# Kernel tuning notes

Hardware: AMD Instinct MI355X
Metric: run time of the kernel (lower is better)

The kernel has to match this reference:

```python
import jax, jax.numpy as jnp
import numpy as np

WS = 8                      # window_size
N = WS * WS                 # 64, Householder dimension
PAD = WS - 1                # reflect-pad total (7)
PAD_LO, PAD_HI = PAD // 2, PAD - PAD // 2  # (3, 4)


def setup_inputs() -> dict:
    key = jax.random.key(0)
    k1, k2 = jax.random.split(key)
    x = jax.random.normal(k1, (2, 8, 256, 256), dtype=jnp.float32)
    v = jax.random.normal(k2, (N, N), dtype=jnp.float32)  # 64 Householder vectors (rows)
    return {"x": x, "v": v}


def _get_A(v):
    # A = prod_i (I - 2 v_i v_i^T / ||v_i||^2), composed left-to-right as in the torch loop.
    # A @ (I - 2 v v^T / s) == A - (2/s) * (A v) v^T  -> rank-1 update per step.
    n = v.shape[-1]
    def step(A, vi):
        s = jnp.sum(vi * vi)
        Av = A @ vi                      # [n]
        return A - (2.0 / s) * jnp.outer(Av, vi), None
    A, _ = jax.lax.scan(step, jnp.eye(n, dtype=v.dtype), v)
    return A


def reference(x, v):
    b, c, H, W = x.shape
    xi = x.reshape(b * c, 1, H, W)
    # reflect padding (3,4) on both spatial dims, as in F.pad(..., mode='reflect')
    xp = jnp.pad(xi, ((0, 0), (0, 0), (PAD_LO, PAD_HI), (PAD_LO, PAD_HI)), mode='reflect')
    # unfold: kernel=8, stride=1, padding=0 -> [bc, 64, H, W] (C=1 so channel ordering matches torch)
    patches = jax.lax.conv_general_dilated_patches(
        xp, filter_shape=(WS, WS), window_strides=(1, 1), padding='VALID')
    cols = patches.reshape(b * c, N, H * W)          # [bc, 64, L]
    A = _get_A(v)                                     # [64, 64]
    # OrthoT1d(dim=1): transpose(1,-1) @ A, transpose back -> out[b,m,l] = sum_k cols[b,k,l] A[k,m]
    out = jnp.einsum('bkl,km->bml', cols, A)          # [bc, 64, L]
    # rearrange 'b (h w) (k1 k2) -> b (h w) k1 k2' with k1=H, k2=W
    return out.reshape(b * c, N, H, W)
```

## Files before the change

### kernel.cpp

```cpp
#include <hip/hip_runtime.h>

#define HSZ 256
#define WSZ 256
#define BC  16
#define NCH 64
#define PADLO 3

#define TW 64
#define TH 8
#define NTHR 256
#define TR 15
#define TC 71
#define TSTRIDE 80

typedef short bf16x8 __attribute__((ext_vector_type(8)));
typedef float f32x4  __attribute__((ext_vector_type(4)));

__device__ __forceinline__ int reflect_idx(int i) {
    i = (i < 0) ? -i : i;
    i = (i >= HSZ) ? (2 * (HSZ - 1) - i) : i;
    return i;
}

__device__ __forceinline__ unsigned short f2bf(float f) {
    unsigned u = __builtin_bit_cast(unsigned, f);
    u += 0x7FFFu + ((u >> 16) & 1u);
    return (unsigned short)(u >> 16);
}

__global__ void build_A_frags(const float* __restrict__ v,
                              unsigned short* __restrict__ frags) {
    __shared__ float As[64][64];
    const int t = threadIdx.x;
    const int w = t >> 6;
    const int l = t & 63;
    const int r = (w << 4) | (l & 15);
    const int q = l >> 4;

    float row[16];
#pragma unroll
    for (int c = 0; c < 16; ++c) row[c] = (q * 16 + c == r) ? 1.0f : 0.0f;

    for (int i = 0; i < 64; ++i) {
        const f32x4* vp = (const f32x4*)(v + i * 64 + q * 16);
        f32x4 v0 = vp[0], v1 = vp[1], v2 = vp[2], v3 = vp[3];
        float vv[16];
#pragma unroll
        for (int j = 0; j < 4; ++j) { vv[j] = v0[j]; vv[4+j] = v1[j]; vv[8+j] = v2[j]; vv[12+j] = v3[j]; }

        float s0 = 0, s1 = 0, s2 = 0, s3 = 0, a0 = 0, a1 = 0, a2 = 0, a3 = 0;
#pragma unroll
        for (int c = 0; c < 4; ++c) {
            s0 = fmaf(vv[c],      vv[c],      s0);
            s1 = fmaf(vv[4+c],    vv[4+c],    s1);
            s2 = fmaf(vv[8+c],    vv[8+c],    s2);
            s3 = fmaf(vv[12+c],   vv[12+c],   s3);
            a0 = fmaf(row[c],     vv[c],      a0);
            a1 = fmaf(row[4+c],   vv[4+c],    a1);
            a2 = fmaf(row[8+c],   vv[8+c],    a2);
            a3 = fmaf(row[12+c],  vv[12+c],   a3);
        }
        float s  = (s0 + s1) + (s2 + s3);
        float av = (a0 + a1) + (a2 + a3);
        av += __shfl_xor(av, 16); s += __shfl_xor(s, 16);
        av += __shfl_xor(av, 32); s += __shfl_xor(s, 32);

        const float scale = 2.0f * av / s;
#pragma unroll
        for (int c = 0; c < 16; ++c) row[c] = fmaf(-scale, vv[c], row[c]);
    }
#pragma unroll
    for (int c = 0; c < 16; ++c) As[r][q * 16 + c] = row[c];
    __syncthreads();

    const int ln = l & 15, lh = l >> 4;
    const int mb = w;
#pragma unroll
    for (int c2 = 0; c2 < 2; ++c2)
#pragma unroll
        for (int j = 0; j < 8; ++j) {
            float val = As[c2 * 32 + lh * 8 + j][mb * 16 + ln];
            frags[(((mb * 2 + c2) * 64) + l) * 8 + j] = f2bf(val);
        }
}

__global__ __launch_bounds__(256)
void ortho_mfma_kernel(const float* __restrict__ x,
                       const unsigned short* __restrict__ frags,
                       float* __restrict__ out) {
    __shared__ float tile[TR][TSTRIDE];

    const int b  = blockIdx.z;
    const int y0 = blockIdx.y * TH;
    const int x0 = blockIdx.x * TW;
    const float* __restrict__ xb = x + (size_t)b * (HSZ * WSZ);

    const int tx = threadIdx.x;
    const int ty = threadIdx.y;
    const int tid = ty * TW + tx;

    for (int idx = tid; idx < TR * TC; idx += NTHR) {
        const int r  = idx / TC;
        const int c  = idx - r * TC;
        tile[r][c] = xb[reflect_idx(y0 + r - PADLO) * WSZ + reflect_idx(x0 + c - PADLO)];
    }

    const int ln = tx & 15, lh = tx >> 4;

    bf16x8 af[4][2];
#pragma unroll
    for (int mb = 0; mb < 4; ++mb)
#pragma unroll
        for (int c = 0; c < 2; ++c)
            af[mb][c] = *(const bf16x8*)(frags + ((mb * 2 + c) * 64 + tx) * 8);

    __syncthreads();

#pragma unroll
    for (int ry = 0; ry < 2; ++ry) {
        const int tyr = ty * 2 + ry;
        const int y   = y0 + tyr;

        unsigned short bfv[2][16];
#pragma unroll
        for (int c = 0; c < 2; ++c) {
            const f32x4* rp = (const f32x4*)&tile[tyr + 4 * c + lh][4 * ln];
            f32x4 q0 = rp[0], q1 = rp[1], q2 = rp[2], q3 = rp[3];
            float fl[16];
#pragma unroll
            for (int j = 0; j < 4; ++j) { fl[j] = q0[j]; fl[4+j] = q1[j]; fl[8+j] = q2[j]; fl[12+j] = q3[j]; }
#pragma unroll
            for (int j = 0; j < 16; ++j) bfv[c][j] = f2bf(fl[j]);
        }

        bf16x8 bfrag[2][4];
#pragma unroll
        for (int c = 0; c < 2; ++c)
#pragma unroll
            for (int g = 0; g < 4; ++g)
#pragma unroll
                for (int j = 0; j < 8; ++j)
                    bfrag[c][g][j] = (short)bfv[c][g + j];

        float* __restrict__ outb =
            out + (size_t)b * NCH * (HSZ * WSZ) + (size_t)y * WSZ + x0 + 4 * ln;

#pragma unroll
        for (int mb = 0; mb < 4; ++mb) {
            f32x4 acc[4];
#pragma unroll
            for (int g = 0; g < 4; ++g) {
                acc[g] = (f32x4){0.0f, 0.0f, 0.0f, 0.0f};
                acc[g] = __builtin_amdgcn_mfma_f32_16x16x32_bf16(af[mb][0], bfrag[0][g], acc[g], 0, 0, 0);
                acc[g] = __builtin_amdgcn_mfma_f32_16x16x32_bf16(af[mb][1], bfrag[1][g], acc[g], 0, 0, 0);
            }
#pragma unroll
            for (int r = 0; r < 4; ++r) {
                const int ch = mb * 16 + lh * 4 + r;
                f32x4 vv = { acc[0][r], acc[1][r], acc[2][r], acc[3][r] };
                __builtin_nontemporal_store(vv, (f32x4*)&outb[(size_t)ch * (HSZ * WSZ)]);
            }
        }
    }
}

extern "C" void kernel_launch(void* const* d_in, const int* in_sizes, int n_in,
                              void* d_out, int out_size, void* d_ws, size_t ws_size,
                              hipStream_t stream) {
    const float* x = (const float*)d_in[0];
    const float* v = (const float*)d_in[1];
    float* outp = (float*)d_out;
    unsigned short* frags = (unsigned short*)d_ws;

    build_A_frags<<<1, 256, 0, stream>>>(v, frags);

    dim3 grid(WSZ / TW, HSZ / TH, BC);
    dim3 block(TW, TH / 2);
    ortho_mfma_kernel<<<grid, block, 0, stream>>>(x, frags, outp);
}
```

Baseline: 80.47 us.

## Double tile height, pack bf16 pairs and build shifted fragments via word shifts

```diff
diff --git a/kernel.cpp b/kernel.cpp
--- a/kernel.cpp
+++ b/kernel.cpp
@@ -1,4 +1,5 @@
 #include <hip/hip_runtime.h>
+#include <hip/hip_bf16.h>
 
 #define HSZ 256
 #define WSZ 256
@@ -7,14 +8,16 @@
 #define PADLO 3
 
 #define TW 64
-#define TH 8
+#define TH 16
+#define RPW 4
 #define NTHR 256
-#define TR 15
+#define TR (TH + 7)
 #define TC 71
 #define TSTRIDE 80
 
 typedef short bf16x8 __attribute__((ext_vector_type(8)));
 typedef float f32x4  __attribute__((ext_vector_type(4)));
+typedef unsigned int u32x4 __attribute__((ext_vector_type(4)));
 
 __device__ __forceinline__ int reflect_idx(int i) {
     i = (i < 0) ? -i : i;
@@ -26,6 +29,13 @@
     unsigned u = __builtin_bit_cast(unsigned, f);
     u += 0x7FFFu + ((u >> 16) & 1u);
     return (unsigned short)(u >> 16);
+}
+
+__device__ __forceinline__ unsigned pk2(float a, float b) {
+    __hip_bfloat162 h = __float22bfloat162_rn(make_float2(a, b));
+    unsigned r;
+    __builtin_memcpy(&r, &h, sizeof(r));
+    return r;
 }
 
 __global__ void build_A_frags(const float* __restrict__ v,
@@ -51,14 +61,14 @@
         float s0 = 0, s1 = 0, s2 = 0, s3 = 0, a0 = 0, a1 = 0, a2 = 0, a3 = 0;
 #pragma unroll
         for (int c = 0; c < 4; ++c) {
-            s0 = fmaf(vv[c],      vv[c],      s0);
-            s1 = fmaf(vv[4+c],    vv[4+c],    s1);
-            s2 = fmaf(vv[8+c],    vv[8+c],    s2);
-            s3 = fmaf(vv[12+c],   vv[12+c],   s3);
-            a0 = fmaf(row[c],     vv[c],      a0);
-            a1 = fmaf(row[4+c],   vv[4+c],    a1);
-            a2 = fmaf(row[8+c],   vv[8+c],    a2);
-            a3 = fmaf(row[12+c],  vv[12+c],   a3);
+            s0 = fmaf(vv[c],     vv[c],     s0);
+            s1 = fmaf(vv[4+c],   vv[4+c],   s1);
+            s2 = fmaf(vv[8+c],   vv[8+c],   s2);
+            s3 = fmaf(vv[12+c],  vv[12+c],  s3);
+            a0 = fmaf(row[c],    vv[c],     a0);
+            a1 = fmaf(row[4+c],  vv[4+c],   a1);
+            a2 = fmaf(row[8+c],  vv[8+c],   a2);
+            a3 = fmaf(row[12+c], vv[12+c],  a3);
         }
         float s  = (s0 + s1) + (s2 + s3);
         float av = (a0 + a1) + (a2 + a3);
@@ -99,10 +109,23 @@
     const int ty = threadIdx.y;
     const int tid = ty * TW + tx;
 
-    for (int idx = tid; idx < TR * TC; idx += NTHR) {
-        const int r  = idx / TC;
-        const int c  = idx - r * TC;
-        tile[r][c] = xb[reflect_idx(y0 + r - PADLO) * WSZ + reflect_idx(x0 + c - PADLO)];
+    {
+        const int grp = tid >> 4;
+        const int lk  = tid & 15;
+        int gcols[5];
+#pragma unroll
+        for (int k = 0; k < 5; ++k) {
+            const int c = lk + 16 * k;
+            gcols[k] = (c < TC) ? reflect_idx(x0 + c - PADLO) : 0;
+        }
+        for (int r = grp; r < TR; r += 16) {
+            const float* rowp = xb + (size_t)reflect_idx(y0 + r - PADLO) * WSZ;
+#pragma unroll
+            for (int k = 0; k < 5; ++k) {
+                const int c = lk + 16 * k;
+                if (c < TC) tile[r][c] = rowp[gcols[k]];
+            }
+        }
     }
 
     const int ln = tx & 15, lh = tx >> 4;
@@ -117,30 +140,42 @@
     __syncthreads();
 
 #pragma unroll
-    for (int ry = 0; ry < 2; ++ry) {
-        const int tyr = ty * 2 + ry;
+    for (int ry = 0; ry < RPW; ++ry) {
+        const int tyr = ty * RPW + ry;
         const int y   = y0 + tyr;
 
-        unsigned short bfv[2][16];
+        unsigned d[2][6];
 #pragma unroll
         for (int c = 0; c < 2; ++c) {
             const f32x4* rp = (const f32x4*)&tile[tyr + 4 * c + lh][4 * ln];
-            f32x4 q0 = rp[0], q1 = rp[1], q2 = rp[2], q3 = rp[3];
-            float fl[16];
-#pragma unroll
-            for (int j = 0; j < 4; ++j) { fl[j] = q0[j]; fl[4+j] = q1[j]; fl[8+j] = q2[j]; fl[12+j] = q3[j]; }
-#pragma unroll
-            for (int j = 0; j < 16; ++j) bfv[c][j] = f2bf(fl[j]);
-        }
-
-        bf16x8 bfrag[2][4];
-#pragma unroll
-        for (int c = 0; c < 2; ++c)
-#pragma unroll
-            for (int g = 0; g < 4; ++g)
-#pragma unroll
-                for (int j = 0; j < 8; ++j)
-                    bfrag[c][g][j] = (short)bfv[c][g + j];
+            f32x4 q0 = rp[0], q1 = rp[1], q2 = rp[2];
+            d[c][0] = pk2(q0[0], q0[1]);
+            d[c][1] = pk2(q0[2], q0[3]);
+            d[c][2] = pk2(q1[0], q1[1]);
+            d[c][3] = pk2(q1[2], q1[3]);
+            d[c][4] = pk2(q2[0], q2[1]);
+            d[c][5] = pk2(q2[2], q2[3]);
+        }
+
+        bf16x8 bfr[2][4];
+#pragma unroll
+        for (int c = 0; c < 2; ++c) {
+            const unsigned* dc = d[c];
+            u32x4 w0 = { dc[0], dc[1], dc[2], dc[3] };
+            u32x4 w2 = { dc[1], dc[2], dc[3], dc[4] };
+            u32x4 w1 = { (dc[0] >> 16) | (dc[1] << 16),
+                         (dc[1] >> 16) | (dc[2] << 16),
+                         (dc[2] >> 16) | (dc[3] << 16),
+                         (dc[3] >> 16) | (dc[4] << 16) };
+            u32x4 w3 = { (dc[1] >> 16) | (dc[2] << 16),
+                         (dc[2] >> 16) | (dc[3] << 16),
+                         (dc[3] >> 16) | (dc[4] << 16),
+                         (dc[4] >> 16) | (dc[5] << 16) };
+            bfr[c][0] = __builtin_bit_cast(bf16x8, w0);
+            bfr[c][1] = __builtin_bit_cast(bf16x8, w1);
+            bfr[c][2] = __builtin_bit_cast(bf16x8, w2);
+            bfr[c][3] = __builtin_bit_cast(bf16x8, w3);
+        }
 
         float* __restrict__ outb =
             out + (size_t)b * NCH * (HSZ * WSZ) + (size_t)y * WSZ + x0 + 4 * ln;
@@ -151,8 +186,8 @@
 #pragma unroll
             for (int g = 0; g < 4; ++g) {
                 acc[g] = (f32x4){0.0f, 0.0f, 0.0f, 0.0f};
-                acc[g] = __builtin_amdgcn_mfma_f32_16x16x32_bf16(af[mb][0], bfrag[0][g], acc[g], 0, 0, 0);
-                acc[g] = __builtin_amdgcn_mfma_f32_16x16x32_bf16(af[mb][1], bfrag[1][g], acc[g], 0, 0, 0);
+                acc[g] = __builtin_amdgcn_mfma_f32_16x16x32_bf16(af[mb][0], bfr[0][g], acc[g], 0, 0, 0);
+                acc[g] = __builtin_amdgcn_mfma_f32_16x16x32_bf16(af[mb][1], bfr[1][g], acc[g], 0, 0, 0);
             }
 #pragma unroll
             for (int r = 0; r < 4; ++r) {
@@ -175,6 +210,6 @@
     build_A_frags<<<1, 256, 0, stream>>>(v, frags);
 
     dim3 grid(WSZ / TW, HSZ / TH, BC);
-    dim3 block(TW, TH / 2);
+    dim3 block(TW, TH / RPW);
     ortho_mfma_kernel<<<grid, block, 0, stream>>>(x, frags, outp);
 }
```

Measured after the change: 87.57 us. +8.8%, slower.
